# Performance work log

Measured on AMD Instinct MI355X. Metric: run time of the kernel, lower is better.

## Reference

```python
import jax, jax.numpy as jnp
import numpy as np

N_EVENTS = 16384   # original pixel events
D = 128            # input_size
H = 128            # hidden_size
K = 9              # kernel 3x3 -> patch coords
S = 2048           # number of patch sequences
LMAX = 108         # max sequence length
T = 147456         # total patch events = sum(lengths) = 9 * N_EVENTS


def setup_inputs() -> dict:
    key = jax.random.key(0)
    ks = jax.random.split(key, 8)
    events = jax.random.normal(ks[0], (N_EVENTS, D), jnp.float32)
    pos_id = jax.random.randint(ks[1], (T,), 0, K, dtype=jnp.int32)
    orig_event_idx = jax.random.randint(ks[2], (T,), 0, N_EVENTS, dtype=jnp.int32)
    # alternating 36/108 lengths: 1024*36 + 1024*108 = 147456 = T
    lengths = jnp.where(jnp.arange(S) % 2 == 0, 36, 108).astype(jnp.int32)
    std = float(np.sqrt(2.0 / (D + H)))
    scatter_w = jax.random.normal(ks[3], (K, H, D), jnp.float32) * std
    gather_w = jax.random.normal(ks[4], (K, H, H), jnp.float32) * std
    lstm_std = float(1.0 / np.sqrt(H))
    w_ih = jax.random.uniform(ks[5], (4 * H, H), jnp.float32, -lstm_std, lstm_std)
    w_hh = jax.random.uniform(ks[6], (4 * H, H), jnp.float32, -lstm_std, lstm_std)
    ln_g = jnp.ones((H,), jnp.float32)
    ln_b = jnp.zeros((H,), jnp.float32)
    return dict(events=events, scatter_w=scatter_w, gather_w=gather_w,
                w_ih=w_ih, w_hh=w_hh, ln_g=ln_g, ln_b=ln_b,
                pos_id=pos_id, orig_event_idx=orig_event_idx, lengths=lengths)


def _pos_proj(x, W, pos_id):
    # position-indexed projection: out[t] = W[pos_id[t]] @ x[t]
    # loop over small fixed K=9 with masked accumulate (matches the torch loop)
    out = jnp.zeros((x.shape[0], W.shape[1]), x.dtype)
    for k in range(W.shape[0]):
        out = out + jnp.where((pos_id == k)[:, None], x @ W[k].T, 0.0)
    return out


def reference(events, scatter_w, gather_w, w_ih, w_hh, ln_g, ln_b,
              pos_id, orig_event_idx, lengths):
    # scatter events to patch replicas
    x = events[orig_event_idx]                           # [T, D]
    x = _pos_proj(x, scatter_w, pos_id)                  # [T, H]

    # flat (sequence-major) -> padded [S, LMAX, H]
    seq_offsets = jnp.cumsum(lengths) - lengths          # [S]
    seq_ids = jnp.repeat(jnp.arange(S), lengths, total_repeat_length=T)
    pos_in_seq = jnp.arange(T) - seq_offsets[seq_ids]
    padded = jnp.zeros((S, LMAX, H), x.dtype).at[seq_ids, pos_in_seq].set(x)

    # single-layer bias-free LSTM (pytorch gate order i, f, g, o), zero init.
    # zero-padding after each sequence's valid region leaves valid outputs
    # identical to a PackedSequence LSTM.
    def step(carry, xt):                                 # xt: [S, H]
        h, c = carry
        gates = xt @ w_ih.T + h @ w_hh.T                 # [S, 4H]
        i, f, g, o = jnp.split(gates, 4, axis=-1)
        c = jax.nn.sigmoid(f) * c + jax.nn.sigmoid(i) * jnp.tanh(g)
        h = jax.nn.sigmoid(o) * jnp.tanh(c)
        return (h, c), h

    init = (jnp.zeros((S, H), x.dtype), jnp.zeros((S, H), x.dtype))
    _, hs = jax.lax.scan(step, init, jnp.swapaxes(padded, 0, 1))  # [LMAX, S, H]
    o_flat = jnp.swapaxes(hs, 0, 1)[seq_ids, pos_in_seq]          # [T, H]

    o_flat = _pos_proj(o_flat, gather_w, pos_id)                  # [T, H]

    # gather patch events back to pixel events (scatter-add) + residual + LN
    out = jnp.zeros((N_EVENTS, H), x.dtype).at[orig_event_idx].add(o_flat)
    out = out + events                                   # input_proj is None (D == H)
    mu = jnp.mean(out, axis=-1, keepdims=True)
    var = jnp.var(out, axis=-1, keepdims=True)
    out = (out - mu) * jax.lax.rsqrt(var + 1e-5) * ln_g + ln_b
    return out
```

## Files before the change

### kernel.cpp

```cpp
#include <hip/hip_runtime.h>

#define N_EVENTS 16384
#define DIM 128
#define NK 9
#define NSEQ 2048
#define TT 147456
#define CHUNK 64
#define NCHUNK_MAX (TT/CHUNK + NK)
#define NHBLK 576

typedef __attribute__((ext_vector_type(8))) short bf16x8;
typedef __attribute__((ext_vector_type(4))) float f32x4;
typedef __attribute__((ext_vector_type(4))) int i32x4;

#define OFF_EV     0UL
#define OFF_WC     (OFF_EV   + (size_t)N_EVENTS*DIM*2)
#define OFF_SCAT   (OFF_WC   + (size_t)512*256*2)
#define OFF_GATH   (OFF_SCAT + (size_t)NK*DIM*DIM*2)
#define OFF_XS     (OFF_GATH + (size_t)NK*DIM*DIM*2)
#define OFF_HS     (OFF_XS   + (size_t)TT*DIM*2)
#define OFF_KLIST  (OFF_HS   + (size_t)TT*DIM*2)
#define OFF_ECNT   (OFF_KLIST+ (size_t)TT*4)
#define OFF_EOFF   (OFF_ECNT + 16384UL*4)
#define OFF_ECNT2  (OFF_EOFF + 16392UL*4)
#define OFF_ELIST  (OFF_ECNT2+ 16384UL*4)
#define OFF_SEQOFF (OFF_ELIST+ (size_t)TT*4)
#define OFF_GROUP  (OFF_SEQOFF + (size_t)NSEQ*4)
#define OFF_MISC   (OFF_GROUP  + (size_t)NSEQ*4)
#define OFF_BH     (OFF_MISC   + 256UL)

__device__ __forceinline__ short f2b(float f) {
    union { float f; unsigned u; } v; v.f = f;
    unsigned r = (v.u + 0x7FFFu + ((v.u >> 16) & 1u)) >> 16;
    return (short)r;
}
__device__ __forceinline__ float asf(unsigned u) {
    union { unsigned u; float f; } v; v.u = u; return v.f;
}
__device__ __forceinline__ float fsig(float x) {
    return __builtin_amdgcn_rcpf(1.f + __expf(-x));
}
__device__ __forceinline__ float ftanh(float x) {
    return 1.f - 2.f * __builtin_amdgcn_rcpf(__expf(2.f * x) + 1.f);
}

__global__ void convert_kernel(const float* __restrict__ ev, const float* __restrict__ wih,
                               const float* __restrict__ whh, const float* __restrict__ sw,
                               const float* __restrict__ gw,
                               short* __restrict__ evb, short* __restrict__ wcb,
                               short* __restrict__ swb, short* __restrict__ gwb,
                               int* __restrict__ ecnt, int* __restrict__ ecnt2) {
    int idx = blockIdx.x * blockDim.x + threadIdx.x;
    if (idx < N_EVENTS * DIM) evb[idx] = f2b(ev[idx]);
    if (idx < 512 * DIM) {
        int j = idx >> 7, d = idx & 127;
        wcb[j * 256 + d]       = f2b(wih[idx]);
        wcb[j * 256 + 128 + d] = f2b(whh[idx]);
    }
    if (idx < NK * DIM * DIM) { swb[idx] = f2b(sw[idx]); gwb[idx] = f2b(gw[idx]); }
    if (idx < N_EVENTS) { ecnt[idx] = 0; ecnt2[idx] = 0; }
}

__global__ void hist_kernel(const int* __restrict__ pos, const int* __restrict__ orig,
                            int* __restrict__ blockhist, int* __restrict__ ecnt) {
    __shared__ int h[NK];
    int tid = threadIdx.x;
    if (tid < NK) h[tid] = 0;
    __syncthreads();
    int t = blockIdx.x * 256 + tid;
    atomicAdd(&h[pos[t]], 1);
    atomicAdd(&ecnt[orig[t]], 1);
    __syncthreads();
    if (tid < NK) blockhist[blockIdx.x * NK + tid] = h[tid];
}

__global__ void plan_kernel(int* __restrict__ blockhist, int* __restrict__ misc,
                            const int* __restrict__ lengths, int* __restrict__ seq_off,
                            int* __restrict__ grouped,
                            const int* __restrict__ ecnt, int* __restrict__ eoff) {
    int tid = threadIdx.x;
    if (blockIdx.x == 0) {
        __shared__ int h[NHBLK * NK];
        for (int i = tid; i < NHBLK * NK; i += 256) h[i] = blockhist[i];
        __syncthreads();
        if (tid < NK) {
            int run = 0;
            for (int b = 0; b < NHBLK; b++) {
                int v = h[b * NK + tid];
                h[b * NK + tid] = run;
                run += v;
            }
            misc[tid] = run;
        }
        __syncthreads();
        if (tid == 0) {
            int ko = 0, co = 0;
            for (int k = 0; k < NK; k++) {
                int c = misc[k];
                misc[32 + k] = ko;
                misc[48 + k] = co;
                ko += c;
                co += (c + CHUNK - 1) / CHUNK;
            }
            misc[48 + NK] = co;
        }
        __syncthreads();
        for (int i = tid; i < NHBLK * NK; i += 256) blockhist[i] = h[i];
    } else if (blockIdx.x == 1) {
        __shared__ int lens[NSEQ];
        __shared__ int tsum[256], tlong[256];
        for (int i = tid; i < NSEQ; i += 256) lens[i] = lengths[i];
        __syncthreads();
        int base = tid * 8;
        int ls[8]; int s = 0, lc = 0;
        #pragma unroll
        for (int i = 0; i < 8; i++) { ls[i] = lens[base + i]; s += ls[i]; lc += (ls[i] > 64) ? 1 : 0; }
        tsum[tid] = s; tlong[tid] = lc;
        __syncthreads();
        for (int d = 1; d < 256; d <<= 1) {
            int a = (tid >= d) ? tsum[tid - d] : 0;
            int b = (tid >= d) ? tlong[tid - d] : 0;
            __syncthreads();
            tsum[tid] += a; tlong[tid] += b;
            __syncthreads();
        }
        int nlong_total = tlong[255];
        int excl = tsum[tid] - s;
        int excl_long = tlong[tid] - lc;
        int run = 0, runl = 0;
        #pragma unroll
        for (int i = 0; i < 8; i++) {
            int sid = base + i;
            seq_off[sid] = excl + run;
            int lb = excl_long + runl;
            if (ls[i] > 64) { grouped[lb] = sid; runl++; }
            else            { grouped[nlong_total + (sid - lb)] = sid; }
            run += ls[i];
        }
    } else {
        __shared__ int part[256];
        int base = tid * 64;
        int s = 0;
        for (int j = 0; j < 64; j++) s += ecnt[base + j];
        part[tid] = s;
        __syncthreads();
        for (int d = 1; d < 256; d <<= 1) {
            int a = (tid >= d) ? part[tid - d] : 0;
            __syncthreads();
            part[tid] += a;
            __syncthreads();
        }
        int run = part[tid] - s;
        for (int j = 0; j < 64; j++) {
            eoff[base + j] = run;
            run += ecnt[base + j];
        }
        if (tid == 255) eoff[N_EVENTS] = run;
    }
}

__global__ void fill_kernel(const int* __restrict__ pos, const int* __restrict__ orig,
                            const int* __restrict__ blockhist, const int* __restrict__ misc,
                            int* __restrict__ klist,
                            const int* __restrict__ eoff, int* __restrict__ ecnt2,
                            int* __restrict__ elist) {
    __shared__ int off[NK];
    int tid = threadIdx.x;
    if (tid < NK) off[tid] = misc[32 + tid] + blockhist[blockIdx.x * NK + tid];
    __syncthreads();
    int t = blockIdx.x * 256 + tid;
    int p = atomicAdd(&off[pos[t]], 1);
    klist[p] = t;
    int o = orig[t];
    int p2 = atomicAdd(&ecnt2[o], 1);
    elist[eoff[o] + p2] = t;
}

__global__ void bucket_gemm(const short* __restrict__ src, const short* __restrict__ wall,
                            const int* __restrict__ klist, const int* __restrict__ misc,
                            const int* __restrict__ orig, short* __restrict__ rows_out,
                            int mode) {
    const int* chunkoff = misc + 48;
    int b = blockIdx.x;
    if (b >= chunkoff[NK]) return;
    int k = 0;
    while (k < NK - 1 && chunkoff[k + 1] <= b) k++;
    int lc = b - chunkoff[k];
    int cnt = misc[k];
    int base = misc[32 + k] + lc * CHUNK;
    int nv = min(CHUNK, cnt - lc * CHUNK);

    __shared__ int tok[CHUNK], ridx[CHUNK];
    __shared__ short A[CHUNK * 136];
    int tid = threadIdx.x;
    if (tid < CHUNK) {
        int tv = klist[base + ((tid < nv) ? tid : 0)];
        tok[tid] = tv;
        ridx[tid] = (mode == 0) ? orig[tv] : tv;
    }
    __syncthreads();
    {
        int row = tid >> 2, part = tid & 3;
        const i32x4* s4 = (const i32x4*)(src + (size_t)ridx[row] * DIM + part * 32);
        i32x4* d4 = (i32x4*)(A + row * 136 + part * 32);
        d4[0] = s4[0]; d4[1] = s4[1]; d4[2] = s4[2]; d4[3] = s4[3];
    }
    __syncthreads();
    int wave = tid >> 6, lane = tid & 63, l15 = lane & 15, q = lane >> 4;
    const short* wk = wall + (size_t)k * DIM * DIM;
    bf16x8 Bf[2][4];
    #pragma unroll
    for (int nt = 0; nt < 2; nt++) {
        int h = wave * 32 + nt * 16 + l15;
        #pragma unroll
        for (int kt = 0; kt < 4; kt++)
            Bf[nt][kt] = *(const bf16x8*)(wk + h * DIM + kt * 32 + q * 8);
    }
    f32x4 C[4][2];
    #pragma unroll
    for (int mt = 0; mt < 4; mt++)
        #pragma unroll
        for (int nt = 0; nt < 2; nt++) C[mt][nt] = (f32x4){0.f, 0.f, 0.f, 0.f};
    #pragma unroll
    for (int mt = 0; mt < 4; mt++) {
        bf16x8 Afr[4];
        const short* ar = A + (mt * 16 + l15) * 136 + q * 8;
        Afr[0] = *(const bf16x8*)(ar);
        Afr[1] = *(const bf16x8*)(ar + 32);
        Afr[2] = *(const bf16x8*)(ar + 64);
        Afr[3] = *(const bf16x8*)(ar + 96);
        #pragma unroll
        for (int nt = 0; nt < 2; nt++)
            #pragma unroll
            for (int kt = 0; kt < 4; kt++)
                C[mt][nt] = __builtin_amdgcn_mfma_f32_16x16x32_bf16(Afr[kt], Bf[nt][kt], C[mt][nt], 0, 0, 0);
    }
    __syncthreads();
    #pragma unroll
    for (int mt = 0; mt < 4; mt++)
        #pragma unroll
        for (int nt = 0; nt < 2; nt++)
            #pragma unroll
            for (int r = 0; r < 4; r++) {
                int row = mt * 16 + q * 4 + r;
                int col = wave * 32 + nt * 16 + l15;
                A[row * 136 + col] = f2b(C[mt][nt][r]);
            }
    __syncthreads();
    {
        int row = tid >> 2, part = tid & 3;
        if (row < nv) {
            const i32x4* s4 = (const i32x4*)(A + row * 136 + part * 32);
            i32x4* d4 = (i32x4*)(rows_out + (size_t)tok[row] * DIM + part * 32);
            d4[0] = s4[0]; d4[1] = s4[1]; d4[2] = s4[2]; d4[3] = s4[3];
        }
    }
}

#define MF(a, b, c) __builtin_amdgcn_mfma_f32_16x16x32_bf16(a, b, c, 0, 0, 0)

#define LSTM_STEP(J, PF) { \
    const int i_ = ib8 + (J); \
    f32x4 Cxi = {0.f,0.f,0.f,0.f}, Cxf = {0.f,0.f,0.f,0.f}; \
    f32x4 Cxg = {0.f,0.f,0.f,0.f}, Cxo = {0.f,0.f,0.f,0.f}; \
    Cxi = MF(PF[0], Bf[0][0], Cxi); Cxf = MF(PF[0], Bf[1][0], Cxf); \
    Cxg = MF(PF[0], Bf[2][0], Cxg); Cxo = MF(PF[0], Bf[3][0], Cxo); \
    Cxi = MF(PF[1], Bf[0][1], Cxi); Cxf = MF(PF[1], Bf[1][1], Cxf); \
    Cxg = MF(PF[1], Bf[2][1], Cxg); Cxo = MF(PF[1], Bf[3][1], Cxo); \
    Cxi = MF(PF[2], Bf[0][2], Cxi); Cxf = MF(PF[2], Bf[1][2], Cxf); \
    Cxg = MF(PF[2], Bf[2][2], Cxg); Cxo = MF(PF[2], Bf[3][2], Cxo); \
    Cxi = MF(PF[3], Bf[0][3], Cxi); Cxf = MF(PF[3], Bf[1][3], Cxf); \
    Cxg = MF(PF[3], Bf[2][3], Cxg); Cxo = MF(PF[3], Bf[3][3], Cxo); \
    bf16x8 Hf0, Hf1, Hf2, Hf3; \
    { const short* hp_ = hb + (((J) + 7) & 7) * 1088 + l15 * 136 + ql * 8; \
      Hf0 = *(const bf16x8*)(hp_);      Hf1 = *(const bf16x8*)(hp_ + 32); \
      Hf2 = *(const bf16x8*)(hp_ + 64); Hf3 = *(const bf16x8*)(hp_ + 96); } \
    f32x4 Chi = {0.f,0.f,0.f,0.f}, Chf = {0.f,0.f,0.f,0.f}; \
    f32x4 Chg = {0.f,0.f,0.f,0.f}, Cho = {0.f,0.f,0.f,0.f}; \
    Chi = MF(Hf0, Bf[0][4], Chi); Chf = MF(Hf0, Bf[1][4], Chf); \
    Chg = MF(Hf0, Bf[2][4], Chg); Cho = MF(Hf0, Bf[3][4], Cho); \
    Chi = MF(Hf1, Bf[0][5], Chi); Chf = MF(Hf1, Bf[1][5], Chf); \
    Chg = MF(Hf1, Bf[2][5], Chg); Cho = MF(Hf1, Bf[3][5], Cho); \
    Chi = MF(Hf2, Bf[0][6], Chi); Chf = MF(Hf2, Bf[1][6], Chf); \
    Chg = MF(Hf2, Bf[2][6], Chg); Cho = MF(Hf2, Bf[3][6], Cho); \
    Chi = MF(Hf3, Bf[0][7], Chi); Chf = MF(Hf3, Bf[1][7], Chf); \
    Chg = MF(Hf3, Bf[2][7], Chg); Cho = MF(Hf3, Bf[3][7], Cho); \
    if (l15 < 8) { \
        const short* xp_ = xs + xoff; \
        PF[0] = *(const bf16x8*)(xp_);      PF[1] = *(const bf16x8*)(xp_ + 32); \
        PF[2] = *(const bf16x8*)(xp_ + 64); PF[3] = *(const bf16x8*)(xp_ + 96); \
    } \
    xoff += ((i_ + 4) <= my_len) ? DIM : 0; \
    f32x4 Gi = Cxi + Chi, Gf = Cxf + Chf, Gg = Cxg + Chg, Go = Cxo + Cho; \
    { \
        int src_ = lane & 31; \
        float i2 = __shfl(Gi[2], src_, 64), i3 = __shfl(Gi[3], src_, 64); \
        float f2 = __shfl(Gf[2], src_, 64), f3 = __shfl(Gf[3], src_, 64); \
        float g2 = __shfl(Gg[2], src_, 64), g3 = __shfl(Gg[3], src_, 64); \
        float o2 = __shfl(Go[2], src_, 64), o3 = __shfl(Go[3], src_, 64); \
        float iA = lo ? Gi[0] : i2, iB = lo ? Gi[1] : i3; \
        float fA = lo ? Gf[0] : f2, fB = lo ? Gf[1] : f3; \
        float gA = lo ? Gg[0] : g2, gB = lo ? Gg[1] : g3; \
        float oA = lo ? Go[0] : o2, oB = lo ? Go[1] : o3; \
        if (i_ < lenA) { \
            float si = fsig(iA), sf = fsig(fA), so = fsig(oA); \
            float tg = ftanh(gA); \
            float cn = sf * cA + si * tg; \
            float th = ftanh(cn); \
            cA = cn; \
            hb[(J) * 1088 + rowA * 136 + u] = f2b(so * th); \
        } \
        if (i_ < lenB) { \
            float si = fsig(iB), sf = fsig(fB), so = fsig(oB); \
            float tg = ftanh(gB); \
            float cn = sf * cB + si * tg; \
            float th = ftanh(cn); \
            cB = cn; \
            hb[(J) * 1088 + rowB * 136 + u] = f2b(so * th); \
        } \
    } \
    __syncthreads(); \
}

__global__ __launch_bounds__(512, 2) void lstm_kernel(
        const short* __restrict__ xs, const short* __restrict__ wc,
        short* __restrict__ hstore, const int* __restrict__ seq_off,
        const int* __restrict__ grouped, const int* __restrict__ lengths) {
    __shared__ int s_off[8], s_len[8];
    __shared__ short hchunk[11][8][136];
    int tid = threadIdx.x;
    if (tid < 8) {
        int s = grouped[blockIdx.x * 8 + tid];
        s_off[tid] = seq_off[s];
        s_len[tid] = lengths[s];
    }
    for (int j = tid; j < 11 * 8 * 136; j += 512) ((short*)hchunk)[j] = 0;
    __syncthreads();
    int lane = tid & 63, l15 = lane & 15, ql = lane >> 4;
    int wave = tid >> 6;
    int u = wave * 16 + l15;
    short* hb = (short*)hchunk;
    bf16x8 Bf[4][8];
    #pragma unroll
    for (int g = 0; g < 4; g++) {
        int j = g * 128 + u;
        #pragma unroll
        for (int kt = 0; kt < 8; kt++)
            Bf[g][kt] = *(const bf16x8*)(wc + j * 256 + kt * 32 + ql * 8);
    }
    int maxlen = 0;
    #pragma unroll
    for (int i = 0; i < 8; i++) maxlen = max(maxlen, s_len[i]);
    int my_off = (l15 < 8) ? s_off[l15] : 0;
    int my_len = (l15 < 8) ? s_len[l15] : 1;
    bool lo = (ql < 2);
    int rowA = lo ? (ql * 4 + 0) : ((ql - 2) * 4 + 2);
    int rowB = lo ? (ql * 4 + 1) : ((ql - 2) * 4 + 3);
    int lenA = s_len[rowA], lenB = s_len[rowB];
    float cA = 0.f, cB = 0.f;
    bf16x8 Pf0[4], Pf1[4];
    #pragma unroll
    for (int k = 0; k < 4; k++) { Pf0[k] = (bf16x8){0,0,0,0,0,0,0,0}; Pf1[k] = Pf0[k]; }
    int xoff = my_off * DIM + ql * 8;
    if (l15 < 8) {
        const short* xp = xs + xoff;
        Pf0[0] = *(const bf16x8*)(xp);      Pf0[1] = *(const bf16x8*)(xp + 32);
        Pf0[2] = *(const bf16x8*)(xp + 64); Pf0[3] = *(const bf16x8*)(xp + 96);
    }
    int xoff1 = xoff + ((my_len > 1) ? DIM : 0);
    if (l15 < 8) {
        const short* xp = xs + xoff1;
        Pf1[0] = *(const bf16x8*)(xp);      Pf1[1] = *(const bf16x8*)(xp + 32);
        Pf1[2] = *(const bf16x8*)(xp + 64); Pf1[3] = *(const bf16x8*)(xp + 96);
    }
    xoff = xoff1 + ((my_len > 2) ? DIM : 0);

    int nb8 = (maxlen + 7) >> 3;
    for (int ob = 0; ob < nb8; ob++) {
        int ib8 = ob * 8;
        LSTM_STEP(0, Pf0)
        LSTM_STEP(1, Pf1)
        LSTM_STEP(2, Pf0)
        LSTM_STEP(3, Pf1)
        LSTM_STEP(4, Pf0)
        LSTM_STEP(5, Pf1)
        LSTM_STEP(6, Pf0)
        LSTM_STEP(7, Pf1)
        #pragma unroll
        for (int it = 0; it < 2; it++) {
            int idx = tid + it * 512;
            int st = idx >> 7, s = (idx >> 4) & 7, part = idx & 15;
            int ig = ib8 + st;
            if (ig < s_len[s]) {
                i32x4 v = *(const i32x4*)&hchunk[st][s][part * 8];
                *(i32x4*)(hstore + (size_t)(s_off[s] + ig) * DIM + part * 8) = v;
            }
        }
        __syncthreads();
    }
}

__global__ void gather_ln(const short* __restrict__ of, const int* __restrict__ eoff,
                          const int* __restrict__ elist, const float* __restrict__ ev,
                          const float* __restrict__ g, const float* __restrict__ bta,
                          float* __restrict__ out) {
    int tid = threadIdx.x;
    int wave = tid >> 6, lane = tid & 63;
    int e = blockIdx.x * 4 + wave;
    int s0 = eoff[e], s1 = eoff[e + 1];
    float x0 = 0.f, x1 = 0.f;
    for (int j = s0; j < s1; j++) {
        int t = elist[j];
        unsigned v = *(const unsigned*)(of + (size_t)t * DIM + lane * 2);
        x0 += asf(v << 16);
        x1 += asf(v & 0xffff0000u);
    }
    const float2* e2 = (const float2*)(ev + (size_t)e * DIM);
    float2 evv = e2[lane];
    x0 += evv.x; x1 += evv.y;
    float sm = x0 + x1, sq = x0 * x0 + x1 * x1;
    #pragma unroll
    for (int m = 1; m < 64; m <<= 1) {
        sm += __shfl_xor(sm, m, 64);
        sq += __shfl_xor(sq, m, 64);
    }
    float mean = sm * (1.f / DIM);
    float var = sq * (1.f / DIM) - mean * mean;
    float rs = rsqrtf(var + 1e-5f);
    float2 gv = ((const float2*)g)[lane], bv = ((const float2*)bta)[lane];
    float2 ov;
    ov.x = (x0 - mean) * rs * gv.x + bv.x;
    ov.y = (x1 - mean) * rs * gv.y + bv.y;
    ((float2*)(out + (size_t)e * DIM))[lane] = ov;
}

extern "C" void kernel_launch(void* const* d_in, const int* in_sizes, int n_in,
                              void* d_out, int out_size, void* d_ws, size_t ws_size,
                              hipStream_t stream) {
    const float* events = (const float*)d_in[0];
    const float* scat   = (const float*)d_in[1];
    const float* gath   = (const float*)d_in[2];
    const float* wih    = (const float*)d_in[3];
    const float* whh    = (const float*)d_in[4];
    const float* lng    = (const float*)d_in[5];
    const float* lnb    = (const float*)d_in[6];
    const int* posid    = (const int*)d_in[7];
    const int* orig     = (const int*)d_in[8];
    const int* lens     = (const int*)d_in[9];
    char* ws = (char*)d_ws;
    short* evb   = (short*)(ws + OFF_EV);
    short* wcb   = (short*)(ws + OFF_WC);
    short* swb   = (short*)(ws + OFF_SCAT);
    short* gwb   = (short*)(ws + OFF_GATH);
    short* xs    = (short*)(ws + OFF_XS);
    short* hs    = (short*)(ws + OFF_HS);
    int*   klist = (int*)(ws + OFF_KLIST);
    int*   ecnt  = (int*)(ws + OFF_ECNT);
    int*   eoff  = (int*)(ws + OFF_EOFF);
    int*   ecnt2 = (int*)(ws + OFF_ECNT2);
    int*   elist = (int*)(ws + OFF_ELIST);
    int*   seqo  = (int*)(ws + OFF_SEQOFF);
    int*   grp   = (int*)(ws + OFF_GROUP);
    int*   misc  = (int*)(ws + OFF_MISC);
    int*   bh    = (int*)(ws + OFF_BH);
    float* out   = (float*)d_out;

    convert_kernel<<<8192, 256, 0, stream>>>(events, wih, whh, scat, gath,
                                             evb, wcb, swb, gwb, ecnt, ecnt2);
    hist_kernel<<<NHBLK, 256, 0, stream>>>(posid, orig, bh, ecnt);
    plan_kernel<<<3, 256, 0, stream>>>(bh, misc, lens, seqo, grp, ecnt, eoff);
    fill_kernel<<<NHBLK, 256, 0, stream>>>(posid, orig, bh, misc, klist, eoff, ecnt2, elist);
    bucket_gemm<<<NCHUNK_MAX, 256, 0, stream>>>(evb, swb, klist, misc, orig, xs, 0);
    lstm_kernel<<<256, 512, 0, stream>>>(xs, wcb, hs, seqo, grp, lens);
    bucket_gemm<<<NCHUNK_MAX, 256, 0, stream>>>(hs, gwb, klist, misc, orig, xs, 1);
    gather_ln<<<4096, 256, 0, stream>>>(xs, eoff, elist, events, lng, lnb, out);
}
```

Baseline: 300.3 us.

## Write gather GEMM output in event-sorted order and fuse convert with histogram

The second position GEMM now scatters rows directly into event-sorted positions using a per-token rank. This lets the final gather+LayerNorm read contiguous rows instead of going through an index list. The convert and position-histogram kernels are merged to save a launch. The per-event count moves into a single plan block using a packed 16-bit LDS histogram, which serialises 147K atomics in one block.

```diff
diff --git a/kernel.cpp b/kernel.cpp
--- a/kernel.cpp
+++ b/kernel.cpp
@@ -20,11 +20,10 @@
 #define OFF_XS     (OFF_GATH + (size_t)NK*DIM*DIM*2)
 #define OFF_HS     (OFF_XS   + (size_t)TT*DIM*2)
 #define OFF_KLIST  (OFF_HS   + (size_t)TT*DIM*2)
-#define OFF_ECNT   (OFF_KLIST+ (size_t)TT*4)
-#define OFF_EOFF   (OFF_ECNT + 16384UL*4)
+#define OFF_EOFF   (OFF_KLIST+ (size_t)TT*4)
 #define OFF_ECNT2  (OFF_EOFF + 16392UL*4)
-#define OFF_ELIST  (OFF_ECNT2+ 16384UL*4)
-#define OFF_SEQOFF (OFF_ELIST+ (size_t)TT*4)
+#define OFF_RANK   (OFF_ECNT2+ 16384UL*4)
+#define OFF_SEQOFF (OFF_RANK + (size_t)TT*4)
 #define OFF_GROUP  (OFF_SEQOFF + (size_t)NSEQ*4)
 #define OFF_MISC   (OFF_GROUP  + (size_t)NSEQ*4)
 #define OFF_BH     (OFF_MISC   + 256UL)
@@ -44,32 +43,27 @@
     return 1.f - 2.f * __builtin_amdgcn_rcpf(__expf(2.f * x) + 1.f);
 }
 
-__global__ void convert_kernel(const float* __restrict__ ev, const float* __restrict__ wih,
-                               const float* __restrict__ whh, const float* __restrict__ sw,
-                               const float* __restrict__ gw,
-                               short* __restrict__ evb, short* __restrict__ wcb,
-                               short* __restrict__ swb, short* __restrict__ gwb,
-                               int* __restrict__ ecnt, int* __restrict__ ecnt2) {
-    int idx = blockIdx.x * blockDim.x + threadIdx.x;
-    if (idx < N_EVENTS * DIM) evb[idx] = f2b(ev[idx]);
-    if (idx < 512 * DIM) {
-        int j = idx >> 7, d = idx & 127;
-        wcb[j * 256 + d]       = f2b(wih[idx]);
-        wcb[j * 256 + 128 + d] = f2b(whh[idx]);
-    }
-    if (idx < NK * DIM * DIM) { swb[idx] = f2b(sw[idx]); gwb[idx] = f2b(gw[idx]); }
-    if (idx < N_EVENTS) { ecnt[idx] = 0; ecnt2[idx] = 0; }
-}
-
-__global__ void hist_kernel(const int* __restrict__ pos, const int* __restrict__ orig,
-                            int* __restrict__ blockhist, int* __restrict__ ecnt) {
+__global__ void convhist_kernel(const float* __restrict__ ev, const float* __restrict__ wih,
+                                const float* __restrict__ whh, const float* __restrict__ sw,
+                                const float* __restrict__ gw, const int* __restrict__ pos,
+                                short* __restrict__ evb, short* __restrict__ wcb,
+                                short* __restrict__ swb, short* __restrict__ gwb,
+                                int* __restrict__ ecnt2, int* __restrict__ blockhist) {
+    int tid = threadIdx.x;
+    int gid = blockIdx.x * 256 + tid;
+    swb[gid] = f2b(sw[gid]);
+    gwb[gid] = f2b(gw[gid]);
+    for (int i = gid; i < N_EVENTS * DIM; i += NHBLK * 256) evb[i] = f2b(ev[i]);
+    if (gid < 512 * DIM) {
+        int j = gid >> 7, d = gid & 127;
+        wcb[j * 256 + d]       = f2b(wih[gid]);
+        wcb[j * 256 + 128 + d] = f2b(whh[gid]);
+    }
+    if (gid < N_EVENTS) ecnt2[gid] = 0;
     __shared__ int h[NK];
-    int tid = threadIdx.x;
     if (tid < NK) h[tid] = 0;
     __syncthreads();
-    int t = blockIdx.x * 256 + tid;
-    atomicAdd(&h[pos[t]], 1);
-    atomicAdd(&ecnt[orig[t]], 1);
+    atomicAdd(&h[pos[gid]], 1);
     __syncthreads();
     if (tid < NK) blockhist[blockIdx.x * NK + tid] = h[tid];
 }
@@ -77,10 +71,11 @@
 __global__ void plan_kernel(int* __restrict__ blockhist, int* __restrict__ misc,
                             const int* __restrict__ lengths, int* __restrict__ seq_off,
                             int* __restrict__ grouped,
-                            const int* __restrict__ ecnt, int* __restrict__ eoff) {
+                            const int* __restrict__ orig, int* __restrict__ eoff) {
+    __shared__ int shbuf[8448];
     int tid = threadIdx.x;
     if (blockIdx.x == 0) {
-        __shared__ int h[NHBLK * NK];
+        int* h = shbuf;
         for (int i = tid; i < NHBLK * NK; i += 256) h[i] = blockhist[i];
         __syncthreads();
         if (tid < NK) {
@@ -107,8 +102,9 @@
         __syncthreads();
         for (int i = tid; i < NHBLK * NK; i += 256) blockhist[i] = h[i];
     } else if (blockIdx.x == 1) {
-        __shared__ int lens[NSEQ];
-        __shared__ int tsum[256], tlong[256];
+        int* lens = shbuf;
+        int* tsum = shbuf + 2048;
+        int* tlong = shbuf + 2304;
         for (int i = tid; i < NSEQ; i += 256) lens[i] = lengths[i];
         __syncthreads();
         int base = tid * 8;
@@ -138,10 +134,21 @@
             run += ls[i];
         }
     } else {
-        __shared__ int part[256];
+        unsigned* eh = (unsigned*)shbuf;
+        int* part = shbuf + 8192;
+        for (int i = tid; i < 8192; i += 256) eh[i] = 0;
+        __syncthreads();
+        for (int j = tid; j < TT; j += 256) {
+            int o = orig[j];
+            atomicAdd(&eh[o >> 1], 1u << ((o & 1) << 4));
+        }
+        __syncthreads();
         int base = tid * 64;
         int s = 0;
-        for (int j = 0; j < 64; j++) s += ecnt[base + j];
+        for (int j = 0; j < 64; j++) {
+            int o = base + j;
+            s += (eh[o >> 1] >> ((o & 1) << 4)) & 0xffff;
+        }
         part[tid] = s;
         __syncthreads();
         for (int d = 1; d < 256; d <<= 1) {
@@ -152,8 +159,9 @@
         }
         int run = part[tid] - s;
         for (int j = 0; j < 64; j++) {
-            eoff[base + j] = run;
-            run += ecnt[base + j];
+            int o = base + j;
+            eoff[o] = run;
+            run += (eh[o >> 1] >> ((o & 1) << 4)) & 0xffff;
         }
         if (tid == 255) eoff[N_EVENTS] = run;
     }
@@ -163,7 +171,7 @@
                             const int* __restrict__ blockhist, const int* __restrict__ misc,
                             int* __restrict__ klist,
                             const int* __restrict__ eoff, int* __restrict__ ecnt2,
-                            int* __restrict__ elist) {
+                            int* __restrict__ rank) {
     __shared__ int off[NK];
     int tid = threadIdx.x;
     if (tid < NK) off[tid] = misc[32 + tid] + blockhist[blockIdx.x * NK + tid];
@@ -173,13 +181,13 @@
     klist[p] = t;
     int o = orig[t];
     int p2 = atomicAdd(&ecnt2[o], 1);
-    elist[eoff[o] + p2] = t;
+    rank[t] = eoff[o] + p2;
 }
 
 __global__ void bucket_gemm(const short* __restrict__ src, const short* __restrict__ wall,
                             const int* __restrict__ klist, const int* __restrict__ misc,
-                            const int* __restrict__ orig, short* __restrict__ rows_out,
-                            int mode) {
+                            const int* __restrict__ orig, const int* __restrict__ rank,
+                            short* __restrict__ rows_out, int mode) {
     const int* chunkoff = misc + 48;
     int b = blockIdx.x;
     if (b >= chunkoff[NK]) return;
@@ -190,12 +198,12 @@
     int base = misc[32 + k] + lc * CHUNK;
     int nv = min(CHUNK, cnt - lc * CHUNK);
 
-    __shared__ int tok[CHUNK], ridx[CHUNK];
+    __shared__ int otok[CHUNK], ridx[CHUNK];
     __shared__ short A[CHUNK * 136];
     int tid = threadIdx.x;
     if (tid < CHUNK) {
         int tv = klist[base + ((tid < nv) ? tid : 0)];
-        tok[tid] = tv;
+        otok[tid] = (mode == 0) ? tv : rank[tv];
         ridx[tid] = (mode == 0) ? orig[tv] : tv;
     }
     __syncthreads();
@@ -251,7 +259,7 @@
         int row = tid >> 2, part = tid & 3;
         if (row < nv) {
             const i32x4* s4 = (const i32x4*)(A + row * 136 + part * 32);
-            i32x4* d4 = (i32x4*)(rows_out + (size_t)tok[row] * DIM + part * 32);
+            i32x4* d4 = (i32x4*)(rows_out + (size_t)otok[row] * DIM + part * 32);
             d4[0] = s4[0]; d4[1] = s4[1]; d4[2] = s4[2]; d4[3] = s4[3];
         }
     }
@@ -401,7 +409,7 @@
 }
 
 __global__ void gather_ln(const short* __restrict__ of, const int* __restrict__ eoff,
-                          const int* __restrict__ elist, const float* __restrict__ ev,
+                          const float* __restrict__ ev,
                           const float* __restrict__ g, const float* __restrict__ bta,
                           float* __restrict__ out) {
     int tid = threadIdx.x;
@@ -410,8 +418,7 @@
     int s0 = eoff[e], s1 = eoff[e + 1];
     float x0 = 0.f, x1 = 0.f;
     for (int j = s0; j < s1; j++) {
-        int t = elist[j];
-        unsigned v = *(const unsigned*)(of + (size_t)t * DIM + lane * 2);
+        unsigned v = *(const unsigned*)(of + (size_t)j * DIM + lane * 2);
         x0 += asf(v << 16);
         x1 += asf(v & 0xffff0000u);
     }
@@ -455,23 +462,21 @@
     short* xs    = (short*)(ws + OFF_XS);
     short* hs    = (short*)(ws + OFF_HS);
     int*   klist = (int*)(ws + OFF_KLIST);
-    int*   ecnt  = (int*)(ws + OFF_ECNT);
     int*   eoff  = (int*)(ws + OFF_EOFF);
     int*   ecnt2 = (int*)(ws + OFF_ECNT2);
-    int*   elist = (int*)(ws + OFF_ELIST);
+    int*   rank  = (int*)(ws + OFF_RANK);
     int*   seqo  = (int*)(ws + OFF_SEQOFF);
     int*   grp   = (int*)(ws + OFF_GROUP);
     int*   misc  = (int*)(ws + OFF_MISC);
     int*   bh    = (int*)(ws + OFF_BH);
     float* out   = (float*)d_out;
 
-    convert_kernel<<<8192, 256, 0, stream>>>(events, wih, whh, scat, gath,
-                                             evb, wcb, swb, gwb, ecnt, ecnt2);
-    hist_kernel<<<NHBLK, 256, 0, stream>>>(posid, orig, bh, ecnt);
-    plan_kernel<<<3, 256, 0, stream>>>(bh, misc, lens, seqo, grp, ecnt, eoff);
-    fill_kernel<<<NHBLK, 256, 0, stream>>>(posid, orig, bh, misc, klist, eoff, ecnt2, elist);
-    bucket_gemm<<<NCHUNK_MAX, 256, 0, stream>>>(evb, swb, klist, misc, orig, xs, 0);
+    convhist_kernel<<<NHBLK, 256, 0, stream>>>(events, wih, whh, scat, gath, posid,
+                                               evb, wcb, swb, gwb, ecnt2, bh);
+    plan_kernel<<<3, 256, 0, stream>>>(bh, misc, lens, seqo, grp, orig, eoff);
+    fill_kernel<<<NHBLK, 256, 0, stream>>>(posid, orig, bh, misc, klist, eoff, ecnt2, rank);
+    bucket_gemm<<<NCHUNK_MAX, 256, 0, stream>>>(evb, swb, klist, misc, orig, rank, xs, 0);
     lstm_kernel<<<256, 512, 0, stream>>>(xs, wcb, hs, seqo, grp, lens);
-    bucket_gemm<<<NCHUNK_MAX, 256, 0, stream>>>(hs, gwb, klist, misc, orig, xs, 1);
-    gather_ln<<<4096, 256, 0, stream>>>(xs, eoff, elist, events, lng, lnb, out);
-}
+    bucket_gemm<<<NCHUNK_MAX, 256, 0, stream>>>(hs, gwb, klist, misc, orig, rank, xs, 1);
+    gather_ln<<<4096, 256, 0, stream>>>(xs, eoff, events, lng, lnb, out);
+}
```

Result: slower. 437.0 us (+45.5%).
